# Optimization experiments

Measured on AMD Instinct MI355X. Metric: run time of the kernel, lower is better.

The kernel has to match this reference:

```python
import jax, jax.numpy as jnp
import numpy as np

IMAGE_SIZE = 800
OUT = 50          # feature map size
FEAT = 512
SCALES = (2.0, 4.0, 6.0)
RATIOS = (0.5, 1.0, 1.5)
A = len(SCALES) * len(RATIOS)          # 9 anchors per cell
POS_THR, NEG_THR = 0.7, 0.3
W_CONF, W_REG = 1.0, 5.0
SCALE = IMAGE_SIZE // OUT              # 16, stride of feature map


def _anchor_base():
    # order: ratio outer loop, scale inner loop (matches get_anchor_base)
    ws = jnp.array([s * r for r in RATIOS for s in SCALES], jnp.float32)  # [A]
    hs = jnp.array([s for r in RATIOS for s in SCALES], jnp.float32)      # [A]
    cx = (jnp.arange(OUT, dtype=jnp.float32) + 0.5)[:, None, None]        # grid dim0 -> x
    cy = (jnp.arange(OUT, dtype=jnp.float32) + 0.5)[None, :, None]        # grid dim1 -> y
    xmin = jnp.clip(cx - ws / 2, 0.0, OUT)
    xmax = jnp.clip(cx + ws / 2, 0.0, OUT)
    ymin = jnp.clip(cy - hs / 2, 0.0, OUT)
    ymax = jnp.clip(cy + hs / 2, 0.0, OUT)
    shp = (OUT, OUT, A)
    base = jnp.stack([jnp.broadcast_to(xmin, shp), jnp.broadcast_to(ymin, shp),
                      jnp.broadcast_to(xmax, shp), jnp.broadcast_to(ymax, shp)], axis=-1)
    return base.reshape(-1, 4)         # [N,4], N = OUT*OUT*A = 22500


def _iou(anchors, gt):
    # anchors [N,4], gt [B,M,4] (xyxy) -> iou [B,N,M]
    a = anchors[None, :, None, :]
    g = gt[:, None, :, :]
    ix1 = jnp.maximum(a[..., 0], g[..., 0]); iy1 = jnp.maximum(a[..., 1], g[..., 1])
    ix2 = jnp.minimum(a[..., 2], g[..., 2]); iy2 = jnp.minimum(a[..., 3], g[..., 3])
    inter = jnp.clip(ix2 - ix1, 0.0) * jnp.clip(iy2 - iy1, 0.0)
    area_a = (a[..., 2] - a[..., 0]) * (a[..., 3] - a[..., 1])
    area_g = (g[..., 2] - g[..., 0]) * (g[..., 3] - g[..., 1])
    return inter / (area_a + area_g - inter + 1e-8)


def _smooth_l1(d):
    ad = jnp.abs(d)
    return jnp.where(ad < 1.0, 0.5 * d * d, ad - 0.5)


def setup_inputs() -> dict:
    key = jax.random.key(0)
    ks = jax.random.split(key, 8)
    B, M = 16, 16
    features = jax.random.normal(ks[0], (B, FEAT, OUT, OUT), jnp.float32)
    # valid GT boxes in image coords: centers in [100,700], sizes in [32,200]
    cxy = jax.random.uniform(ks[1], (B, M, 2), jnp.float32, 100.0, 700.0)
    wh = jax.random.uniform(ks[2], (B, M, 2), jnp.float32, 32.0, 200.0)
    x1y1 = jnp.clip(cxy - wh / 2, 0.0, IMAGE_SIZE)
    x2y2 = jnp.clip(cxy + wh / 2, 0.0, IMAGE_SIZE)
    gt_boxes = jnp.concatenate([x1y1, x2y2], axis=-1)
    w1 = jax.random.normal(ks[3], (FEAT, FEAT, 3, 3), jnp.float32) * 0.02
    b1 = jnp.zeros((FEAT,), jnp.float32)
    w_cls = jax.random.normal(ks[4], (A, FEAT), jnp.float32) * 0.02
    b_cls = jnp.zeros((A,), jnp.float32)
    w_box = jax.random.normal(ks[5], (4 * A, FEAT), jnp.float32) * 0.02
    b_box = jnp.zeros((4 * A,), jnp.float32)
    return {"features": features, "gt_boxes": gt_boxes, "w1": w1, "b1": b1,
            "w_cls": w_cls, "b_cls": b_cls, "w_box": w_box, "b_box": b_box}


def reference(features, gt_boxes, w1, b1, w_cls, b_cls, w_box, b_box):
    B = features.shape[0]
    anchors = _anchor_base()                                   # [N,4]
    N = anchors.shape[0]

    # --- conv tower ---
    x = jax.lax.conv_general_dilated(features, w1, (1, 1), 'SAME') + b1[None, :, None, None]
    cls_map = jnp.einsum('bchw,ac->bahw', x, w_cls) + b_cls[None, :, None, None]   # [B,A,H,W]
    box_map = jnp.einsum('bchw,dc->bdhw', x, w_box) + b_box[None, :, None, None]   # [B,4A,H,W]
    logits = jnp.transpose(cls_map, (0, 2, 3, 1)).reshape(B, N)                    # [B,N]
    pred_off = jnp.transpose(box_map.reshape(B, A, 4, OUT, OUT), (0, 3, 4, 1, 2)).reshape(B, N, 4)

    # --- project gt to feature-map (anchor) coords, 'p2a' ---
    gt = gt_boxes / SCALE                                       # [B,M,4]

    # --- anchor/GT assignment ---
    iou = _iou(anchors, gt)                                     # [B,N,M]
    max_per_gt = jnp.max(iou, axis=1, keepdims=True)            # best anchor per gt
    pos_mask = ((iou == max_per_gt) & (max_per_gt > 0)) | (iou > POS_THR)  # [B,N,M]
    pos_mask = pos_mask.astype(jnp.float32)
    n_pos = jnp.maximum(pos_mask.sum(), 1.0)

    # --- gt offsets (standard tx,ty,tw,th) for every (anchor,gt) pair ---
    acx = (anchors[:, 0] + anchors[:, 2]) / 2
    acy = (anchors[:, 1] + anchors[:, 3]) / 2
    aw = jnp.maximum(anchors[:, 2] - anchors[:, 0], 1e-6)
    ah = jnp.maximum(anchors[:, 3] - anchors[:, 1], 1e-6)
    gcx = (gt[..., 0] + gt[..., 2]) / 2                         # [B,M]
    gcy = (gt[..., 1] + gt[..., 3]) / 2
    gw = jnp.maximum(gt[..., 2] - gt[..., 0], 1e-6)
    gh = jnp.maximum(gt[..., 3] - gt[..., 1], 1e-6)
    tx = (gcx[:, None, :] - acx[None, :, None]) / aw[None, :, None]   # [B,N,M]
    ty = (gcy[:, None, :] - acy[None, :, None]) / ah[None, :, None]
    tw = jnp.log(gw[:, None, :] / aw[None, :, None])
    th = jnp.log(gh[:, None, :] / ah[None, :, None])
    gt_off = jnp.stack([tx, ty, tw, th], axis=-1)               # [B,N,M,4]

    diff = gt_off - pred_off[:, :, None, :]
    reg_loss = (pos_mask[..., None] * _smooth_l1(diff)).sum() / (4.0 * n_pos)

    # --- classification loss: BCE-with-logits; positives=1, negatives=0 ---
    pos_loss = (pos_mask * jax.nn.softplus(-logits)[:, :, None]).sum() / n_pos
    neg_anchor = jnp.all(iou < NEG_THR, axis=2).astype(jnp.float32)   # [B,N]
    n_neg = jnp.maximum(neg_anchor.sum(), 1.0)
    neg_loss = (neg_anchor * jax.nn.softplus(logits)).sum() / n_neg
    cls_loss = 0.5 * (pos_loss + neg_loss)

    total_rpn_loss = W_CONF * cls_loss + W_REG * reg_loss

    # --- proposals from predicted offsets for all anchors ---
    pcx = acx[None, :] + pred_off[..., 0] * aw[None, :]
    pcy = acy[None, :] + pred_off[..., 1] * ah[None, :]
    pw = aw[None, :] * jnp.exp(pred_off[..., 2])
    ph = ah[None, :] * jnp.exp(pred_off[..., 3])
    proposals = jnp.stack([pcx - pw / 2, pcy - ph / 2, pcx + pw / 2, pcy + ph / 2], axis=-1)  # [B,N,4]

    return total_rpn_loss, proposals
```

## Files before the change

kernel.cpp:

```cpp
#include <hip/hip_runtime.h>
#include <hip/hip_bf16.h>
#include <stdint.h>


using bf16x8 = __attribute__((ext_vector_type(8))) __bf16;
using f32x4  = __attribute__((ext_vector_type(4))) float;

#define FT_CHUNK_STRIDE 2768896
#define W2_CHUNK_B 27648

__device__ __forceinline__ unsigned short f2bf(float f) {
  union { float f; unsigned u; } x; x.f = f;
  unsigned r = x.u + 0x7fffu + ((x.u >> 16) & 1u);
  return (unsigned short)(r >> 16);
}

__device__ __forceinline__ void gl_lds16(const void* g, void* l) {
  __builtin_amdgcn_global_load_lds(
      (const __attribute__((address_space(1))) void*)g,
      (__attribute__((address_space(3))) void*)l, 16, 0, 0);
}

__device__ __forceinline__ float sl1(float d) {
  float ad = fabsf(d);
  return ad < 1.f ? 0.5f * d * d : ad - 0.5f;
}
__device__ __forceinline__ float softplus_f(float x) {
  return fmaxf(x, 0.f) + log1pf(expf(-fabsf(x)));
}

__device__ __forceinline__ void anchor_strict(int n, float& ax1, float& ay1,
                                              float& ax2, float& ay2) {
  int ii = n / 450;
  int rem = n - ii * 450;
  int jj = rem / 9;
  int a  = rem - jj * 9;
  const float SC[3] = {2.f, 4.f, 6.f};
  const float RA[3] = {0.5f, 1.f, 1.5f};
  float w = __fmul_rn(SC[a % 3], RA[a / 3]);
  float h = SC[a % 3];
  float cx = __fadd_rn((float)ii, 0.5f);
  float cy = __fadd_rn((float)jj, 0.5f);
  float wh = __fmul_rn(w, 0.5f), hh = __fmul_rn(h, 0.5f);
  ax1 = fminf(fmaxf(__fsub_rn(cx, wh), 0.f), 50.f);
  ax2 = fminf(fmaxf(__fadd_rn(cx, wh), 0.f), 50.f);
  ay1 = fminf(fmaxf(__fsub_rn(cy, hh), 0.f), 50.f);
  ay2 = fminf(fmaxf(__fadd_rn(cy, hh), 0.f), 50.f);
}
__device__ __forceinline__ float iou_strict(float ax1, float ay1, float ax2, float ay2,
                                            float aarea, const float* __restrict__ g) {
  float gx1 = __fmul_rn(g[0], 0.0625f), gy1 = __fmul_rn(g[1], 0.0625f);
  float gx2 = __fmul_rn(g[2], 0.0625f), gy2 = __fmul_rn(g[3], 0.0625f);
  float ix1 = fmaxf(ax1, gx1), iy1 = fmaxf(ay1, gy1);
  float ix2 = fminf(ax2, gx2), iy2 = fminf(ay2, gy2);
  float inter = __fmul_rn(fmaxf(__fsub_rn(ix2, ix1), 0.f),
                          fmaxf(__fsub_rn(iy2, iy1), 0.f));
  float garea = __fmul_rn(__fsub_rn(gx2, gx1), __fsub_rn(gy2, gy1));
  float denom = __fadd_rn(__fsub_rn(__fadd_rn(aarea, garea), inter), 1e-8f);
  return __fdiv_rn(inter, denom);
}

__global__ __launch_bounds__(256, 4) void k1(const float* __restrict__ feat,
                                             char* __restrict__ featT2,
                                             const float* __restrict__ w1,
                                             const float* __restrict__ wc,
                                             const float* __restrict__ wb,
                                             const float* __restrict__ b1,
                                             const float* __restrict__ bc,
                                             const float* __restrict__ bbx,
                                             float* __restrict__ part,
                                             float* __restrict__ bias_eff,
                                             unsigned* __restrict__ zbuf) {
  __shared__ __align__(16) char smem[128 * 132 * 2];
  const int bxr = blockIdx.x;
  const int tid = threadIdx.x;

  if (bxr < 576) {
    if (bxr == 0) {
      if (tid < 256) zbuf[tid] = 0u;
      if (tid < 8) zbuf[256 + tid] = 0u;
    }
    int cz = bxr / 72, kx = bxr - cz * 72;
    float* sW = (float*)smem;
#pragma unroll
    for (int q = 0; q < 12; ++q) {
      int idx = tid + q * 256;
      int co = idx >> 6, cl = idx & 63;
      int c = cz * 64 + cl;
      float v = 0.f;
      if (co < 9) v = wc[co * 512 + c];
      else if (co < 45) v = wb[(co - 9) * 512 + c];
      sW[co * 64 + cl] = v;
    }
    __syncthreads();
    const int kmem = kx * 64 + (tid & 63);
    const int coq  = tid >> 6;
    float acc[12];
#pragma unroll
    for (int j = 0; j < 12; ++j) acc[j] = 0.f;
    const float* w1p = w1 + (size_t)(cz * 64) * 4608 + kmem;
    for (int c4 = 0; c4 < 64; c4 += 4) {
      float f0 = w1p[(size_t)(c4 + 0) * 4608];
      float f1 = w1p[(size_t)(c4 + 1) * 4608];
      float f2 = w1p[(size_t)(c4 + 2) * 4608];
      float f3 = w1p[(size_t)(c4 + 3) * 4608];
#pragma unroll
      for (int j = 0; j < 12; ++j) {
        float4 wv = *(const float4*)&sW[(coq * 12 + j) * 64 + c4];
        acc[j] += wv.x * f0 + wv.y * f1 + wv.z * f2 + wv.w * f3;
      }
    }
    float* dst = part + (size_t)cz * 221184 + kmem;
#pragma unroll
    for (int j = 0; j < 12; ++j) dst[(size_t)(coq * 12 + j) * 4608] = acc[j];
    return;
  }

  if (bxr < 624) {
    int co = bxr - 576;
    int l = tid;
    if (l >= 64) return;
    float s = 0.f;
#pragma unroll
    for (int q = 0; q < 8; ++q) {
      int c = q * 64 + l;
      float wv = co < 9 ? wc[co * 512 + c] : (co < 45 ? wb[(co - 9) * 512 + c] : 0.f);
      s += wv * b1[c];
    }
    for (int o = 32; o; o >>= 1) s += __shfl_down(s, o, 64);
    if (l == 0)
      bias_eff[co] = s + (co < 9 ? bc[co] : (co < 45 ? bbx[co - 9] : 0.f));
    return;
  }

  const int bxr2 = bxr - 624;
  const int tile = bxr2 % 21;
  const int rest = bxr2 / 21;
  const int g    = rest & 3;
  const int b    = rest >> 2;
  if (tile == 20) {
    uint4 z = {0, 0, 0, 0};
    for (int u = tid; u < 204 * 4; u += 256) {
      int p = u & 255; if (p >= 204) p -= 204;
      int c4 = u / 204;
      int ip, jp;
      if (p < 52)       { ip = 0;       jp = p; }
      else if (p < 104) { ip = 51;      jp = p - 52; }
      else if (p < 154) { ip = p - 103; jp = 0; }
      else              { ip = p - 153; jp = 51; }
      char* dst = featT2 + (size_t)(g * 4 + c4) * FT_CHUNK_STRIDE
                + (size_t)(b * 2704 + ip * 52 + jp) * 64;
      *(uint4*)(dst)      = z;
      *(uint4*)(dst + 16) = z;
      *(uint4*)(dst + 32) = z;
      *(uint4*)(dst + 48) = z;
    }
    return;
  }
  unsigned short* sT = (unsigned short*)smem;
  const int pos0 = tile * 128;
  const float* fb = feat + (size_t)b * 1280000 + (size_t)(g * 128) * 2500;
  const int pq = tid & 31;
  const int rg = tid >> 5;
  const int p  = pos0 + pq * 4;
  float vv[16][4];
  if (p + 3 < 2500) {
#pragma unroll
    for (int it = 0; it < 4; ++it)
#pragma unroll
      for (int q = 0; q < 4; ++q) {
        float4 v = *(const float4*)(fb + (size_t)(it * 32 + rg * 4 + q) * 2500 + p);
        vv[it * 4 + q][0] = v.x; vv[it * 4 + q][1] = v.y;
        vv[it * 4 + q][2] = v.z; vv[it * 4 + q][3] = v.w;
      }
  } else {
#pragma unroll
    for (int it = 0; it < 4; ++it)
#pragma unroll
      for (int q = 0; q < 4; ++q)
#pragma unroll
        for (int e = 0; e < 4; ++e)
          vv[it * 4 + q][e] = fb[(size_t)(it * 32 + rg * 4 + q) * 2500 + min(p + e, 2499)];
  }
#pragma unroll
  for (int it = 0; it < 4; ++it) {
    int cb = it * 32 + rg * 4;
#pragma unroll
    for (int pp = 0; pp < 4; ++pp) {
      ushort4 pk;
      pk.x = f2bf(vv[it * 4 + 0][pp]); pk.y = f2bf(vv[it * 4 + 1][pp]);
      pk.z = f2bf(vv[it * 4 + 2][pp]); pk.w = f2bf(vv[it * 4 + 3][pp]);
      *(ushort4*)&sT[(pq * 4 + pp) * 132 + cb] = pk;
    }
  }
  __syncthreads();
#pragma unroll
  for (int q2 = 0; q2 < 2; ++q2) {
    int u = tid + q2 * 256;
    int ch = u >> 7, pr = u & 127;
    int gp = pos0 + pr;
    if (gp >= 2500) continue;
    int i = gp / 50, j = gp - i * 50;
    char* dst = featT2 + (size_t)(g * 4 + ch) * FT_CHUNK_STRIDE
              + (size_t)(b * 2704 + (i + 1) * 52 + (j + 1)) * 64;
    const uint4* src = (const uint4*)&sT[pr * 132 + ch * 32];
    uint4 a0 = src[0], a1 = src[1], a2 = src[2], a3 = src[3];
    *(uint4*)(dst)      = a0;
    *(uint4*)(dst + 16) = a1;
    *(uint4*)(dst + 32) = a2;
    *(uint4*)(dst + 48) = a3;
  }
}

__global__ __launch_bounds__(256) void k2(const float* __restrict__ part,
                                          unsigned short* __restrict__ w2,
                                          const float* __restrict__ gt_boxes,
                                          unsigned* __restrict__ mx) {
  if (blockIdx.x >= 864) {
    int q = blockIdx.x - 864;
    int b = q / 88, nb = q - b * 88;
    int n = nb * 256 + threadIdx.x;
    float lm[16];
#pragma unroll
    for (int m = 0; m < 16; ++m) lm[m] = 0.f;
    if (n < 22500) {
      float ax1, ay1, ax2, ay2;
      anchor_strict(n, ax1, ay1, ax2, ay2);
      float aarea = __fmul_rn(__fsub_rn(ax2, ax1), __fsub_rn(ay2, ay1));
#pragma unroll
      for (int m = 0; m < 16; ++m)
        lm[m] = iou_strict(ax1, ay1, ax2, ay2, aarea, gt_boxes + (b * 16 + m) * 4);
    }
    __shared__ float red[4][16];
#pragma unroll
    for (int m = 0; m < 16; ++m) {
      float v = lm[m];
      for (int o = 32; o; o >>= 1) v = fmaxf(v, __shfl_down(v, o, 64));
      if ((threadIdx.x & 63) == 0) red[threadIdx.x >> 6][m] = v;
    }
    __syncthreads();
    if (threadIdx.x < 16) {
      float v = fmaxf(fmaxf(red[0][threadIdx.x], red[1][threadIdx.x]),
                      fmaxf(red[2][threadIdx.x], red[3][threadIdx.x]));
      atomicMax(mx + b * 16 + threadIdx.x, __float_as_uint(v));
    }
    return;
  }
  int co = blockIdx.x / 18, kx = blockIdx.x - co * 18;
  int kmem = kx * 256 + threadIdx.x;
  const float* p = part + (size_t)co * 4608 + kmem;
  float s = 0.f;
#pragma unroll
  for (int cz = 0; cz < 8; ++cz) s += p[(size_t)cz * 221184];
  int ci = kmem / 9, tap = kmem - ci * 9;
  int c = ci >> 5, e = ci & 31;
  int boff = c * W2_CHUNK_B + tap * 3072 + (co >> 4) * 1024 + (co & 15) * 64
           + ((((e >> 3) ^ co) & 3) << 4) + ((e & 7) << 1);
  w2[boff >> 1] = f2bf(s);
}

__global__ __launch_bounds__(256, 2) void k3(const char* __restrict__ featT2,
                                             const char* __restrict__ w2g,
                                             const float* __restrict__ beff,
                                             float* __restrict__ oh) {
  __shared__ __align__(16) char sF[2][11264];
  __shared__ __align__(16) char sA[2][27648];
  const int tid = threadIdx.x, lane = tid & 63, w = tid >> 6;
  const int bx0 = blockIdx.x;
  const int bx = ((bx0 & 7) << 6) | (bx0 >> 3);
  const int b = bx >> 5, tl = bx & 31, tr = tl >> 3, tc = tl & 7;
  const int i0 = tr * 13 - (tr == 3 ? 1 : 0);
  const int TI = (tr >= 2) ? 12 : 13;
  const int TJ = (tc < 2) ? 7 : 6;
  const int j0 = (tc < 2) ? tc * 7 : 14 + (tc - 2) * 6;
  const int TJ2 = TJ + 2;
  const int mcount = TI * TJ;
  const int pieces = (TI + 2) * TJ2 * 5;

  const char* srcF[3];
#pragma unroll
  for (int k = 0; k < 3; ++k) {
    int s = w * 3 + k;
    int pi = s * 64 + lane;
    if (pi >= pieces) pi = pieces - 1;
    int pos = pi / 5, pc = pi - pos * 5;
    if (pc > 3) pc = 3;
    int hi = pos / TJ2, hj = pos - hi * TJ2;
    srcF[k] = featT2 + (size_t)(b * 2704 + (i0 + hi) * 52 + (j0 + hj)) * 64 + pc * 16;
  }
  int idxB[2];
#pragma unroll
  for (int bf = 0; bf < 2; ++bf) {
    int p = (w * 2 + bf) * 16 + (lane & 15);
    if (p >= mcount) p = mcount - 1;
    int di = p / TJ, dj = p - di * TJ;
    idxB[bf] = (di * TJ2 + dj) * 80 + (lane >> 4) * 16;
  }
  const int aoff = (lane & 15) * 64 + ((((lane >> 4) ^ lane) & 3) << 4);
  int toff[9];
#pragma unroll
  for (int tp = 0; tp < 9; ++tp) toff[tp] = ((tp / 3) * TJ2 + (tp % 3)) * 80;

  f32x4 acc[3][2] = {};

  auto stage = [&](int c, int pb) {
    size_t coff = (size_t)c * FT_CHUNK_STRIDE;
#pragma unroll
    for (int k = 0; k < 3; ++k) {
      int s = w * 3 + k;
      if (s < 11) gl_lds16(srcF[k] + coff, sF[pb] + s * 1024);
    }
#pragma unroll
    for (int k = 0; k < 7; ++k) {
      int s = w + 4 * k;
      if (s < 27)
        gl_lds16(w2g + (size_t)c * W2_CHUNK_B + s * 1024 + lane * 16, sA[pb] + s * 1024);
    }
  };

  stage(0, 0);
  __builtin_amdgcn_s_waitcnt(0);
  __syncthreads();

  for (int c = 0; c < 16; ++c) {
    int pb = c & 1;
    if (c < 15) stage(c + 1, pb ^ 1);
    const char* fA = sA[pb];
    const char* fB = sF[pb];
#pragma unroll
    for (int tp = 0; tp < 9; ++tp) {
      bf16x8 av[3], bv[2];
#pragma unroll
      for (int cf = 0; cf < 3; ++cf)
        av[cf] = *(const bf16x8*)(fA + tp * 3072 + cf * 1024 + aoff);
#pragma unroll
      for (int bf = 0; bf < 2; ++bf)
        bv[bf] = *(const bf16x8*)(fB + idxB[bf] + toff[tp]);
#pragma unroll
      for (int cf = 0; cf < 3; ++cf)
#pragma unroll
        for (int bf = 0; bf < 2; ++bf)
          acc[cf][bf] = __builtin_amdgcn_mfma_f32_16x16x32_bf16(av[cf], bv[bf], acc[cf][bf], 0, 0, 0);
    }
    __builtin_amdgcn_s_waitcnt(0);
    __syncthreads();
  }

  f32x4 bias[3];
#pragma unroll
  for (int cf = 0; cf < 3; ++cf)
    bias[cf] = *(const f32x4*)(beff + cf * 16 + (lane >> 4) * 4);
#pragma unroll
  for (int bf = 0; bf < 2; ++bf) {
    int p = (w * 2 + bf) * 16 + (lane & 15);
    if (p >= mcount) continue;
    int di = p / TJ, dj = p - di * TJ;
    int gm = (b * 50 + i0 + di) * 50 + (j0 + dj);
#pragma unroll
    for (int cf = 0; cf < 3; ++cf) {
      f32x4 v = acc[cf][bf];
#pragma unroll
      for (int r = 0; r < 4; ++r) v[r] += bias[cf][r];
      *(f32x4*)(oh + (size_t)gm * 48 + cf * 16 + (lane >> 4) * 4) = v;
    }
  }
}

__global__ __launch_bounds__(256) void k4(const float* __restrict__ gt_boxes,
                                          const unsigned* __restrict__ mxbuf,
                                          const float* __restrict__ oh,
                                          float* __restrict__ accum,
                                          float* __restrict__ dout) {
  int b = blockIdx.y;
  int n = blockIdx.x * 256 + threadIdx.x;
  float s_np = 0.f, s_reg = 0.f, s_pos = 0.f, s_nc = 0.f, s_nl = 0.f;
  if (n < 22500) {
    float ax1, ay1, ax2, ay2;
    anchor_strict(n, ax1, ay1, ax2, ay2);
    float aarea = __fmul_rn(__fsub_rn(ax2, ax1), __fsub_rn(ay2, ay1));
    float acx = (ax1 + ax2) * 0.5f, acy = (ay1 + ay2) * 0.5f;
    float aw = fmaxf(ax2 - ax1, 1e-6f), ah = fmaxf(ay2 - ay1, 1e-6f);
    int ii = n / 450, rem = n - ii * 450, jj = rem / 9, a = rem - jj * 9;
    const float* row = oh + ((size_t)(b * 2500 + ii * 50 + jj)) * 48;
    float logit = row[a];
    float p0 = row[9 + a * 4], p1 = row[10 + a * 4];
    float p2 = row[11 + a * 4], p3 = row[12 + a * 4];
    int npos = 0;
    bool allneg = true;
#pragma unroll
    for (int m = 0; m < 16; ++m) {
      const float* g = gt_boxes + (b * 16 + m) * 4;
      float iou = iou_strict(ax1, ay1, ax2, ay2, aarea, g);
      float mxv = __uint_as_float(mxbuf[b * 16 + m]);
      bool pos = ((iou == mxv) && (mxv > 0.f)) || (iou > 0.7f);
      if (iou >= 0.3f) allneg = false;
      if (pos) {
        ++npos;
        float gx1 = g[0] * 0.0625f, gy1 = g[1] * 0.0625f;
        float gx2 = g[2] * 0.0625f, gy2 = g[3] * 0.0625f;
        float gcx = (gx1 + gx2) * 0.5f, gcy = (gy1 + gy2) * 0.5f;
        float gw = fmaxf(gx2 - gx1, 1e-6f), gh = fmaxf(gy2 - gy1, 1e-6f);
        float tx = (gcx - acx) / aw, ty = (gcy - acy) / ah;
        float twv = logf(gw / aw), thv = logf(gh / ah);
        s_reg += sl1(tx - p0) + sl1(ty - p1) + sl1(twv - p2) + sl1(thv - p3);
      }
    }
    s_np = (float)npos;
    s_pos = (float)npos * softplus_f(-logit);
    if (allneg) { s_nc = 1.f; s_nl = softplus_f(logit); }
    float pcx = acx + p0 * aw, pcy = acy + p1 * ah;
    float pw = aw * expf(p2), ph = ah * expf(p3);
    float* o = dout + 1 + ((size_t)b * 22500 + n) * 4;
    o[0] = pcx - pw * 0.5f;
    o[1] = pcy - ph * 0.5f;
    o[2] = pcx + pw * 0.5f;
    o[3] = pcy + ph * 0.5f;
  }
  float vals[5] = {s_np, s_reg, s_pos, s_nc, s_nl};
  __shared__ float red[4][5];
#pragma unroll
  for (int q = 0; q < 5; ++q) {
    float v = vals[q];
    for (int o = 32; o; o >>= 1) v += __shfl_down(v, o, 64);
    if ((threadIdx.x & 63) == 0) red[threadIdx.x >> 6][q] = v;
  }
  __syncthreads();
  if (threadIdx.x < 5) {
    float v = red[0][threadIdx.x] + red[1][threadIdx.x] +
              red[2][threadIdx.x] + red[3][threadIdx.x];
    atomicAdd(accum + threadIdx.x, v);
  }
  __syncthreads();
  if (threadIdx.x == 0) {
    __threadfence();
    unsigned old = atomicAdd((unsigned*)(accum + 5), 1u);
    if (old == 1407u) {
      float np = fmaxf(atomicAdd(accum + 0, 0.f), 1.f);
      float rg = atomicAdd(accum + 1, 0.f);
      float pp = atomicAdd(accum + 2, 0.f);
      float nn = fmaxf(atomicAdd(accum + 3, 0.f), 1.f);
      float nl = atomicAdd(accum + 4, 0.f);
      dout[0] = 0.5f * (pp / np + nl / nn) + 5.f * (rg / (4.f * np));
    }
  }
}

extern "C" void kernel_launch(void* const* d_in, const int* in_sizes, int n_in,
                              void* d_out, int out_size, void* d_ws, size_t ws_size,
                              hipStream_t stream) {
  const float* features = (const float*)d_in[0];
  const float* gt_boxes = (const float*)d_in[1];
  const float* w1    = (const float*)d_in[2];
  const float* b1    = (const float*)d_in[3];
  const float* w_cls = (const float*)d_in[4];
  const float* b_cls = (const float*)d_in[5];
  const float* w_box = (const float*)d_in[6];
  const float* b_box = (const float*)d_in[7];
  float* out = (float*)d_out;
  char* ws = (char*)d_ws;

  char*           featT2 = ws;
  unsigned short* w2     = (unsigned short*)(ws + 44302336);
  float*          wpart  = (float*)(ws + 44855296);
  float*          oh     = (float*)(ws + 51933184);
  float*          beff   = (float*)(ws + 59613184);
  unsigned*       mx     = (unsigned*)(ws + 59613376);
  float*          accum  = (float*)(ws + 59614400);

  k1<<<1968, 256, 0, stream>>>(features, featT2, w1, w_cls, w_box, b1, b_cls,
                               b_box, wpart, beff, mx);
  k2<<<2272, 256, 0, stream>>>(wpart, w2, gt_boxes, mx);
  k3<<<512, 256, 0, stream>>>(featT2, (const char*)w2, beff, oh);
  k4<<<dim3(88, 16), 256, 0, stream>>>(gt_boxes, mx, oh, accum, out);
}
```

Measured before the change: 251.4 us.

## Cache IoU matrix, split transpose kernel, replace atomic max with partial reduction

Splits the old k1 into a feature-transpose kernel with smaller 64-position tiles and a weight/IoU kernel. The IoU pass now writes every per-anchor IoU to a workspace buffer, so k4 reads them back instead of recomputing. Per-block maxima go to a partial array that one k2 block reduces, replacing atomicMax. GT box terms are precomputed in shared memory. This cuts redundant IoU divisions and atomic contention, at the cost of about 23 MB of extra global writes and reads and a changed kernel order.

```diff
diff --git a/kernel.cpp b/kernel.cpp
--- a/kernel.cpp
+++ b/kernel.cpp
@@ -47,98 +47,26 @@
   ay1 = fminf(fmaxf(__fsub_rn(cy, hh), 0.f), 50.f);
   ay2 = fminf(fmaxf(__fadd_rn(cy, hh), 0.f), 50.f);
 }
-__device__ __forceinline__ float iou_strict(float ax1, float ay1, float ax2, float ay2,
-                                            float aarea, const float* __restrict__ g) {
-  float gx1 = __fmul_rn(g[0], 0.0625f), gy1 = __fmul_rn(g[1], 0.0625f);
-  float gx2 = __fmul_rn(g[2], 0.0625f), gy2 = __fmul_rn(g[3], 0.0625f);
-  float ix1 = fmaxf(ax1, gx1), iy1 = fmaxf(ay1, gy1);
-  float ix2 = fminf(ax2, gx2), iy2 = fminf(ay2, gy2);
+__device__ __forceinline__ float iou_pre(float ax1, float ay1, float ax2, float ay2,
+                                         float aarea, const float* __restrict__ s) {
+  float ix1 = fmaxf(ax1, s[0]), iy1 = fmaxf(ay1, s[1]);
+  float ix2 = fminf(ax2, s[2]), iy2 = fminf(ay2, s[3]);
   float inter = __fmul_rn(fmaxf(__fsub_rn(ix2, ix1), 0.f),
                           fmaxf(__fsub_rn(iy2, iy1), 0.f));
-  float garea = __fmul_rn(__fsub_rn(gx2, gx1), __fsub_rn(gy2, gy1));
-  float denom = __fadd_rn(__fsub_rn(__fadd_rn(aarea, garea), inter), 1e-8f);
+  float denom = __fadd_rn(__fsub_rn(__fadd_rn(aarea, s[4]), inter), 1e-8f);
   return __fdiv_rn(inter, denom);
 }
 
-__global__ __launch_bounds__(256, 4) void k1(const float* __restrict__ feat,
-                                             char* __restrict__ featT2,
-                                             const float* __restrict__ w1,
-                                             const float* __restrict__ wc,
-                                             const float* __restrict__ wb,
-                                             const float* __restrict__ b1,
-                                             const float* __restrict__ bc,
-                                             const float* __restrict__ bbx,
-                                             float* __restrict__ part,
-                                             float* __restrict__ bias_eff,
-                                             unsigned* __restrict__ zbuf) {
-  __shared__ __align__(16) char smem[128 * 132 * 2];
-  const int bxr = blockIdx.x;
+__global__ __launch_bounds__(256, 6) void k1a(const float* __restrict__ feat,
+                                              char* __restrict__ featT2) {
+  __shared__ __align__(16) unsigned short sT[64 * 132];
+  const int bx = blockIdx.x;
   const int tid = threadIdx.x;
-
-  if (bxr < 576) {
-    if (bxr == 0) {
-      if (tid < 256) zbuf[tid] = 0u;
-      if (tid < 8) zbuf[256 + tid] = 0u;
-    }
-    int cz = bxr / 72, kx = bxr - cz * 72;
-    float* sW = (float*)smem;
-#pragma unroll
-    for (int q = 0; q < 12; ++q) {
-      int idx = tid + q * 256;
-      int co = idx >> 6, cl = idx & 63;
-      int c = cz * 64 + cl;
-      float v = 0.f;
-      if (co < 9) v = wc[co * 512 + c];
-      else if (co < 45) v = wb[(co - 9) * 512 + c];
-      sW[co * 64 + cl] = v;
-    }
-    __syncthreads();
-    const int kmem = kx * 64 + (tid & 63);
-    const int coq  = tid >> 6;
-    float acc[12];
-#pragma unroll
-    for (int j = 0; j < 12; ++j) acc[j] = 0.f;
-    const float* w1p = w1 + (size_t)(cz * 64) * 4608 + kmem;
-    for (int c4 = 0; c4 < 64; c4 += 4) {
-      float f0 = w1p[(size_t)(c4 + 0) * 4608];
-      float f1 = w1p[(size_t)(c4 + 1) * 4608];
-      float f2 = w1p[(size_t)(c4 + 2) * 4608];
-      float f3 = w1p[(size_t)(c4 + 3) * 4608];
-#pragma unroll
-      for (int j = 0; j < 12; ++j) {
-        float4 wv = *(const float4*)&sW[(coq * 12 + j) * 64 + c4];
-        acc[j] += wv.x * f0 + wv.y * f1 + wv.z * f2 + wv.w * f3;
-      }
-    }
-    float* dst = part + (size_t)cz * 221184 + kmem;
-#pragma unroll
-    for (int j = 0; j < 12; ++j) dst[(size_t)(coq * 12 + j) * 4608] = acc[j];
-    return;
-  }
-
-  if (bxr < 624) {
-    int co = bxr - 576;
-    int l = tid;
-    if (l >= 64) return;
-    float s = 0.f;
-#pragma unroll
-    for (int q = 0; q < 8; ++q) {
-      int c = q * 64 + l;
-      float wv = co < 9 ? wc[co * 512 + c] : (co < 45 ? wb[(co - 9) * 512 + c] : 0.f);
-      s += wv * b1[c];
-    }
-    for (int o = 32; o; o >>= 1) s += __shfl_down(s, o, 64);
-    if (l == 0)
-      bias_eff[co] = s + (co < 9 ? bc[co] : (co < 45 ? bbx[co - 9] : 0.f));
-    return;
-  }
-
-  const int bxr2 = bxr - 624;
-  const int tile = bxr2 % 21;
-  const int rest = bxr2 / 21;
+  const int tile = bx % 41;
+  const int rest = bx / 41;
   const int g    = rest & 3;
   const int b    = rest >> 2;
-  if (tile == 20) {
+  if (tile == 40) {
     uint4 z = {0, 0, 0, 0};
     for (int u = tid; u < 204 * 4; u += 256) {
       int p = u & 255; if (p >= 204) p -= 204;
@@ -157,69 +85,142 @@
     }
     return;
   }
-  unsigned short* sT = (unsigned short*)smem;
-  const int pos0 = tile * 128;
+  const int pos0 = tile * 64;
   const float* fb = feat + (size_t)b * 1280000 + (size_t)(g * 128) * 2500;
-  const int pq = tid & 31;
-  const int rg = tid >> 5;
+  const int pq = tid & 15;
+  const int cq = tid >> 4;
   const int p  = pos0 + pq * 4;
-  float vv[16][4];
+  float vv[2][4][4];
   if (p + 3 < 2500) {
 #pragma unroll
-    for (int it = 0; it < 4; ++it)
+    for (int it = 0; it < 2; ++it)
 #pragma unroll
       for (int q = 0; q < 4; ++q) {
-        float4 v = *(const float4*)(fb + (size_t)(it * 32 + rg * 4 + q) * 2500 + p);
-        vv[it * 4 + q][0] = v.x; vv[it * 4 + q][1] = v.y;
-        vv[it * 4 + q][2] = v.z; vv[it * 4 + q][3] = v.w;
+        float4 v = *(const float4*)(fb + (size_t)(it * 64 + cq * 4 + q) * 2500 + p);
+        vv[it][q][0] = v.x; vv[it][q][1] = v.y;
+        vv[it][q][2] = v.z; vv[it][q][3] = v.w;
       }
   } else {
 #pragma unroll
-    for (int it = 0; it < 4; ++it)
+    for (int it = 0; it < 2; ++it)
 #pragma unroll
       for (int q = 0; q < 4; ++q)
 #pragma unroll
         for (int e = 0; e < 4; ++e)
-          vv[it * 4 + q][e] = fb[(size_t)(it * 32 + rg * 4 + q) * 2500 + min(p + e, 2499)];
-  }
-#pragma unroll
-  for (int it = 0; it < 4; ++it) {
-    int cb = it * 32 + rg * 4;
+          vv[it][q][e] = fb[(size_t)(it * 64 + cq * 4 + q) * 2500 + min(p + e, 2499)];
+  }
+#pragma unroll
+  for (int it = 0; it < 2; ++it) {
 #pragma unroll
     for (int pp = 0; pp < 4; ++pp) {
       ushort4 pk;
-      pk.x = f2bf(vv[it * 4 + 0][pp]); pk.y = f2bf(vv[it * 4 + 1][pp]);
-      pk.z = f2bf(vv[it * 4 + 2][pp]); pk.w = f2bf(vv[it * 4 + 3][pp]);
-      *(ushort4*)&sT[(pq * 4 + pp) * 132 + cb] = pk;
+      pk.x = f2bf(vv[it][0][pp]); pk.y = f2bf(vv[it][1][pp]);
+      pk.z = f2bf(vv[it][2][pp]); pk.w = f2bf(vv[it][3][pp]);
+      *(ushort4*)&sT[(pq * 4 + pp) * 132 + it * 64 + cq * 4] = pk;
     }
   }
   __syncthreads();
-#pragma unroll
-  for (int q2 = 0; q2 < 2; ++q2) {
-    int u = tid + q2 * 256;
-    int ch = u >> 7, pr = u & 127;
+  {
+    int ch = tid >> 6, pr = tid & 63;
     int gp = pos0 + pr;
-    if (gp >= 2500) continue;
-    int i = gp / 50, j = gp - i * 50;
-    char* dst = featT2 + (size_t)(g * 4 + ch) * FT_CHUNK_STRIDE
-              + (size_t)(b * 2704 + (i + 1) * 52 + (j + 1)) * 64;
-    const uint4* src = (const uint4*)&sT[pr * 132 + ch * 32];
-    uint4 a0 = src[0], a1 = src[1], a2 = src[2], a3 = src[3];
-    *(uint4*)(dst)      = a0;
-    *(uint4*)(dst + 16) = a1;
-    *(uint4*)(dst + 32) = a2;
-    *(uint4*)(dst + 48) = a3;
-  }
-}
-
-__global__ __launch_bounds__(256) void k2(const float* __restrict__ part,
-                                          unsigned short* __restrict__ w2,
-                                          const float* __restrict__ gt_boxes,
-                                          unsigned* __restrict__ mx) {
-  if (blockIdx.x >= 864) {
-    int q = blockIdx.x - 864;
+    if (gp < 2500) {
+      int i = gp / 50, j = gp - i * 50;
+      char* dst = featT2 + (size_t)(g * 4 + ch) * FT_CHUNK_STRIDE
+                + (size_t)(b * 2704 + (i + 1) * 52 + (j + 1)) * 64;
+      const uint4* src = (const uint4*)&sT[pr * 132 + ch * 32];
+      uint4 a0 = src[0], a1 = src[1], a2 = src[2], a3 = src[3];
+      *(uint4*)(dst)      = a0;
+      *(uint4*)(dst + 16) = a1;
+      *(uint4*)(dst + 32) = a2;
+      *(uint4*)(dst + 48) = a3;
+    }
+  }
+}
+
+__global__ __launch_bounds__(256, 4) void k1b(const float* __restrict__ w1,
+                                              const float* __restrict__ wc,
+                                              const float* __restrict__ wb,
+                                              const float* __restrict__ b1,
+                                              const float* __restrict__ bc,
+                                              const float* __restrict__ bbx,
+                                              float* __restrict__ part,
+                                              float* __restrict__ bias_eff,
+                                              const float* __restrict__ gt_boxes,
+                                              float* __restrict__ iouBuf,
+                                              float* __restrict__ mxPart,
+                                              unsigned* __restrict__ accz) {
+  __shared__ __align__(16) float sW[48 * 64];
+  const int bxr = blockIdx.x;
+  const int tid = threadIdx.x;
+
+  if (bxr < 576) {
+    if (bxr == 0 && tid < 8) accz[tid] = 0u;
+    int cz = bxr / 72, kx = bxr - cz * 72;
+#pragma unroll
+    for (int q = 0; q < 12; ++q) {
+      int idx = tid + q * 256;
+      int co = idx >> 6, cl = idx & 63;
+      int c = cz * 64 + cl;
+      float v = 0.f;
+      if (co < 9) v = wc[co * 512 + c];
+      else if (co < 45) v = wb[(co - 9) * 512 + c];
+      sW[co * 64 + cl] = v;
+    }
+    __syncthreads();
+    const int kmem = kx * 64 + (tid & 63);
+    const int coq  = tid >> 6;
+    float acc[12];
+#pragma unroll
+    for (int j = 0; j < 12; ++j) acc[j] = 0.f;
+    const float* w1p = w1 + (size_t)(cz * 64) * 4608 + kmem;
+    for (int c4 = 0; c4 < 64; c4 += 4) {
+      float f0 = w1p[(size_t)(c4 + 0) * 4608];
+      float f1 = w1p[(size_t)(c4 + 1) * 4608];
+      float f2 = w1p[(size_t)(c4 + 2) * 4608];
+      float f3 = w1p[(size_t)(c4 + 3) * 4608];
+#pragma unroll
+      for (int j = 0; j < 12; ++j) {
+        float4 wv = *(const float4*)&sW[(coq * 12 + j) * 64 + c4];
+        acc[j] += wv.x * f0 + wv.y * f1 + wv.z * f2 + wv.w * f3;
+      }
+    }
+    float* dst = part + (size_t)cz * 221184 + kmem;
+#pragma unroll
+    for (int j = 0; j < 12; ++j) dst[(size_t)(coq * 12 + j) * 4608] = acc[j];
+    return;
+  }
+
+  if (bxr < 624) {
+    int co = bxr - 576;
+    int l = tid;
+    if (l >= 64) return;
+    float s = 0.f;
+#pragma unroll
+    for (int q = 0; q < 8; ++q) {
+      int c = q * 64 + l;
+      float wv = co < 9 ? wc[co * 512 + c] : (co < 45 ? wb[(co - 9) * 512 + c] : 0.f);
+      s += wv * b1[c];
+    }
+    for (int o = 32; o; o >>= 1) s += __shfl_down(s, o, 64);
+    if (l == 0)
+      bias_eff[co] = s + (co < 9 ? bc[co] : (co < 45 ? bbx[co - 9] : 0.f));
+    return;
+  }
+
+  {
+    int q = bxr - 624;
     int b = q / 88, nb = q - b * 88;
-    int n = nb * 256 + threadIdx.x;
+    int n = nb * 256 + tid;
+    float (*sgg)[5] = (float(*)[5])sW;
+    float (*red)[16] = (float(*)[16])(sW + 128);
+    if (tid < 16) {
+      const float* g = gt_boxes + (b * 16 + tid) * 4;
+      float gx1 = __fmul_rn(g[0], 0.0625f), gy1 = __fmul_rn(g[1], 0.0625f);
+      float gx2 = __fmul_rn(g[2], 0.0625f), gy2 = __fmul_rn(g[3], 0.0625f);
+      sgg[tid][0] = gx1; sgg[tid][1] = gy1; sgg[tid][2] = gx2; sgg[tid][3] = gy2;
+      sgg[tid][4] = __fmul_rn(__fsub_rn(gx2, gx1), __fsub_rn(gy2, gy1));
+    }
+    __syncthreads();
     float lm[16];
 #pragma unroll
     for (int m = 0; m < 16; ++m) lm[m] = 0.f;
@@ -229,21 +230,41 @@
       float aarea = __fmul_rn(__fsub_rn(ax2, ax1), __fsub_rn(ay2, ay1));
 #pragma unroll
       for (int m = 0; m < 16; ++m)
-        lm[m] = iou_strict(ax1, ay1, ax2, ay2, aarea, gt_boxes + (b * 16 + m) * 4);
-    }
-    __shared__ float red[4][16];
+        lm[m] = iou_pre(ax1, ay1, ax2, ay2, aarea, sgg[m]);
+      float* dv = iouBuf + (size_t)(b * 22500 + n) * 16;
+#pragma unroll
+      for (int v4 = 0; v4 < 4; ++v4) {
+        float4 pk;
+        pk.x = lm[v4 * 4 + 0]; pk.y = lm[v4 * 4 + 1];
+        pk.z = lm[v4 * 4 + 2]; pk.w = lm[v4 * 4 + 3];
+        *(float4*)(dv + v4 * 4) = pk;
+      }
+    }
 #pragma unroll
     for (int m = 0; m < 16; ++m) {
       float v = lm[m];
       for (int o = 32; o; o >>= 1) v = fmaxf(v, __shfl_down(v, o, 64));
-      if ((threadIdx.x & 63) == 0) red[threadIdx.x >> 6][m] = v;
+      if ((tid & 63) == 0) red[tid >> 6][m] = v;
     }
     __syncthreads();
-    if (threadIdx.x < 16) {
-      float v = fmaxf(fmaxf(red[0][threadIdx.x], red[1][threadIdx.x]),
-                      fmaxf(red[2][threadIdx.x], red[3][threadIdx.x]));
-      atomicMax(mx + b * 16 + threadIdx.x, __float_as_uint(v));
-    }
+    if (tid < 16) {
+      float v = fmaxf(fmaxf(red[0][tid], red[1][tid]),
+                      fmaxf(red[2][tid], red[3][tid]));
+      mxPart[(b * 16 + tid) * 88 + nb] = v;
+    }
+  }
+}
+
+__global__ __launch_bounds__(256) void k2(const float* __restrict__ part,
+                                          unsigned short* __restrict__ w2,
+                                          const float* __restrict__ mxPart,
+                                          unsigned* __restrict__ mx) {
+  if (blockIdx.x == 864) {
+    int t = threadIdx.x;
+    const float* mp = mxPart + t * 88;
+    float v = 0.f;
+    for (int k = 0; k < 88; ++k) v = fmaxf(v, mp[k]);
+    mx[t] = __float_as_uint(v);
     return;
   }
   int co = blockIdx.x / 18, kx = blockIdx.x - co * 18;
@@ -366,18 +387,32 @@
   }
 }
 
-__global__ __launch_bounds__(256) void k4(const float* __restrict__ gt_boxes,
-                                          const unsigned* __restrict__ mxbuf,
-                                          const float* __restrict__ oh,
-                                          float* __restrict__ accum,
-                                          float* __restrict__ dout) {
-  int b = blockIdx.y;
-  int n = blockIdx.x * 256 + threadIdx.x;
+__global__ __launch_bounds__(256, 2) void k4(const float* __restrict__ gt_boxes,
+                                             const unsigned* __restrict__ mxbuf,
+                                             const float* __restrict__ iouBuf,
+                                             const float* __restrict__ oh,
+                                             float* __restrict__ accum,
+                                             float* __restrict__ dout) {
+  const int tid = threadIdx.x;
+  const int b = blockIdx.y;
+  __shared__ float sg[16][5];
+  if (tid < 16) {
+    const float* g = gt_boxes + (b * 16 + tid) * 4;
+    float gx1 = __fmul_rn(g[0], 0.0625f), gy1 = __fmul_rn(g[1], 0.0625f);
+    float gx2 = __fmul_rn(g[2], 0.0625f), gy2 = __fmul_rn(g[3], 0.0625f);
+    sg[tid][0] = (gx1 + gx2) * 0.5f;
+    sg[tid][1] = (gy1 + gy2) * 0.5f;
+    sg[tid][2] = fmaxf(gx2 - gx1, 1e-6f);
+    sg[tid][3] = fmaxf(gy2 - gy1, 1e-6f);
+    sg[tid][4] = __uint_as_float(mxbuf[b * 16 + tid]);
+  }
+  __syncthreads();
+
+  const int n = blockIdx.x * 256 + tid;
   float s_np = 0.f, s_reg = 0.f, s_pos = 0.f, s_nc = 0.f, s_nl = 0.f;
   if (n < 22500) {
     float ax1, ay1, ax2, ay2;
     anchor_strict(n, ax1, ay1, ax2, ay2);
-    float aarea = __fmul_rn(__fsub_rn(ax2, ax1), __fsub_rn(ay2, ay1));
     float acx = (ax1 + ax2) * 0.5f, acy = (ay1 + ay2) * 0.5f;
     float aw = fmaxf(ax2 - ax1, 1e-6f), ah = fmaxf(ay2 - ay1, 1e-6f);
     int ii = n / 450, rem = n - ii * 450, jj = rem / 9, a = rem - jj * 9;
@@ -385,23 +420,26 @@
     float logit = row[a];
     float p0 = row[9 + a * 4], p1 = row[10 + a * 4];
     float p2 = row[11 + a * 4], p3 = row[12 + a * 4];
+    const float* iv = iouBuf + (size_t)(b * 22500 + n) * 16;
+    float io[16];
+#pragma unroll
+    for (int v4 = 0; v4 < 4; ++v4) {
+      float4 v = *(const float4*)(iv + v4 * 4);
+      io[v4 * 4 + 0] = v.x; io[v4 * 4 + 1] = v.y;
+      io[v4 * 4 + 2] = v.z; io[v4 * 4 + 3] = v.w;
+    }
     int npos = 0;
     bool allneg = true;
 #pragma unroll
     for (int m = 0; m < 16; ++m) {
-      const float* g = gt_boxes + (b * 16 + m) * 4;
-      float iou = iou_strict(ax1, ay1, ax2, ay2, aarea, g);
-      float mxv = __uint_as_float(mxbuf[b * 16 + m]);
+      float iou = io[m];
+      float mxv = sg[m][4];
       bool pos = ((iou == mxv) && (mxv > 0.f)) || (iou > 0.7f);
       if (iou >= 0.3f) allneg = false;
       if (pos) {
         ++npos;
-        float gx1 = g[0] * 0.0625f, gy1 = g[1] * 0.0625f;
-        float gx2 = g[2] * 0.0625f, gy2 = g[3] * 0.0625f;
-        float gcx = (gx1 + gx2) * 0.5f, gcy = (gy1 + gy2) * 0.5f;
-        float gw = fmaxf(gx2 - gx1, 1e-6f), gh = fmaxf(gy2 - gy1, 1e-6f);
-        float tx = (gcx - acx) / aw, ty = (gcy - acy) / ah;
-        float twv = logf(gw / aw), thv = logf(gh / ah);
+        float tx = (sg[m][0] - acx) / aw, ty = (sg[m][1] - acy) / ah;
+        float twv = logf(sg[m][2] / aw), thv = logf(sg[m][3] / ah);
         s_reg += sl1(tx - p0) + sl1(ty - p1) + sl1(twv - p2) + sl1(thv - p3);
       }
     }
@@ -422,16 +460,15 @@
   for (int q = 0; q < 5; ++q) {
     float v = vals[q];
     for (int o = 32; o; o >>= 1) v += __shfl_down(v, o, 64);
-    if ((threadIdx.x & 63) == 0) red[threadIdx.x >> 6][q] = v;
+    if ((tid & 63) == 0) red[tid >> 6][q] = v;
   }
   __syncthreads();
-  if (threadIdx.x < 5) {
-    float v = red[0][threadIdx.x] + red[1][threadIdx.x] +
-              red[2][threadIdx.x] + red[3][threadIdx.x];
-    atomicAdd(accum + threadIdx.x, v);
+  if (tid < 5) {
+    float v = red[0][tid] + red[1][tid] + red[2][tid] + red[3][tid];
+    atomicAdd(accum + tid, v);
   }
   __syncthreads();
-  if (threadIdx.x == 0) {
+  if (tid == 0) {
     __threadfence();
     unsigned old = atomicAdd((unsigned*)(accum + 5), 1u);
     if (old == 1407u) {
@@ -464,12 +501,15 @@
   float*          wpart  = (float*)(ws + 44855296);
   float*          oh     = (float*)(ws + 51933184);
   float*          beff   = (float*)(ws + 59613184);
-  unsigned*       mx     = (unsigned*)(ws + 59613376);
-  float*          accum  = (float*)(ws + 59614400);
-
-  k1<<<1968, 256, 0, stream>>>(features, featT2, w1, w_cls, w_box, b1, b_cls,
-                               b_box, wpart, beff, mx);
-  k2<<<2272, 256, 0, stream>>>(wpart, w2, gt_boxes, mx);
+  float*          mxPart = (float*)(ws + 59613376);
+  unsigned*       mx     = (unsigned*)(ws + 59703488);
+  float*          accum  = (float*)(ws + 59704512);
+  float*          iouBuf = (float*)(ws + 59704576);
+
+  k1b<<<2032, 256, 0, stream>>>(w1, w_cls, w_box, b1, b_cls, b_box, wpart, beff,
+                                gt_boxes, iouBuf, mxPart, (unsigned*)accum);
+  k2<<<865, 256, 0, stream>>>(wpart, w2, mxPart, mx);
+  k1a<<<2624, 256, 0, stream>>>(features, featT2);
   k3<<<512, 256, 0, stream>>>(featT2, (const char*)w2, beff, oh);
-  k4<<<dim3(88, 16), 256, 0, stream>>>(gt_boxes, mx, oh, accum, out);
-}
+  k4<<<dim3(88, 16), 256, 0, stream>>>(gt_boxes, mx, iouBuf, oh, accum, out);
+}
```

Result: slower. 291.2 us (+15.8%).
